# Kernel optimization log

Hardware: AMD Instinct MI355X
Metric: run time of the kernel (lower is better)

## Reference

```python
import jax, jax.numpy as jnp
import numpy as np
import math

PATCH = 41
NUM_ANG = 8
NUM_SPATIAL = 4
BIN_KSIZE = 2 * int(PATCH / (NUM_SPATIAL + 1))   # 16
BIN_STRIDE = PATCH // NUM_SPATIAL                # 10
BIN_PAD = BIN_KSIZE // 4                         # 4
CLIPVAL = 0.2
EPS = 1e-10
N = 8192


def _sift_pooling_kernel(ksize: int) -> np.ndarray:
    k2 = float(ksize) / 2.0
    xc2 = k2 - np.abs(np.arange(ksize, dtype=np.float32) + 0.5 - k2)
    return (np.outer(xc2, xc2) / k2 ** 2).astype(np.float32)


def _sift_weighting_kernel(ksize: int) -> np.ndarray:
    # Gauss, vlfeat sigma: sigma_mul_2 = ksize**2
    k2 = float(ksize) / 2.0
    ys = np.arange(ksize, dtype=np.float32)[:, None]
    xs = np.arange(ksize, dtype=np.float32)[None, :]
    disq = (ys - k2 + 0.5) ** 2 + (xs - k2 + 0.5) ** 2
    return np.exp(-disq / float(ksize ** 2)).astype(np.float32)


def setup_inputs() -> dict:
    key = jax.random.key(0)
    x = jax.random.normal(key, (N, 1, PATCH, PATCH), dtype=jnp.float32)
    gk = jnp.asarray(_sift_weighting_kernel(PATCH))   # [41,41]
    pk = jnp.asarray(_sift_pooling_kernel(BIN_KSIZE))  # [16,16]
    return {"x": x, "gk": gk, "pk": pk}


def _l2_normalize(v):
    return v / jnp.maximum(jnp.linalg.norm(v, axis=1, keepdims=True), 1e-12)


def reference(x, gk, pk):
    # gradients via replicate-pad + central difference (matches [-1,0,1] convs)
    xp = jnp.pad(x, ((0, 0), (0, 0), (0, 0), (1, 1)), mode='edge')
    gx = xp[..., 2:] - xp[..., :-2]
    yp = jnp.pad(x, ((0, 0), (0, 0), (1, 1), (0, 0)), mode='edge')
    gy = yp[:, :, 2:, :] - yp[:, :, :-2, :]

    mag = jnp.sqrt(gx * gx + gy * gy + EPS) * gk  # gaussian-weighted magnitude
    ori = jnp.arctan2(gy, gx + EPS)

    # soft angular binning
    o_big = (ori + 2.0 * math.pi) / (2.0 * math.pi) * NUM_ANG
    bo0f = jnp.floor(o_big)
    wo1 = o_big - bo0f
    bo0 = bo0f.astype(jnp.int32) % NUM_ANG
    bo1 = (bo0 + 1) % NUM_ANG
    # [N,1,P,P,nb]
    contrib = (jax.nn.one_hot(bo0, NUM_ANG, dtype=mag.dtype) * ((1.0 - wo1) * mag)[..., None]
               + jax.nn.one_hot(bo1, NUM_ANG, dtype=mag.dtype) * (wo1 * mag)[..., None])
    contrib = jnp.transpose(contrib[:, 0], (0, 3, 1, 2))  # [N,nb,P,P]

    # depthwise weighted spatial pooling (same triangular kernel per angular bin)
    kern = jnp.broadcast_to(pk[None, None], (NUM_ANG, 1, BIN_KSIZE, BIN_KSIZE))
    pooled = jax.lax.conv_general_dilated(
        contrib, kern,
        window_strides=(BIN_STRIDE, BIN_STRIDE),
        padding=[(BIN_PAD, BIN_PAD), (BIN_PAD, BIN_PAD)],
        feature_group_count=NUM_ANG,
        dimension_numbers=('NCHW', 'OIHW', 'NCHW'))  # [N,nb,4,4]

    desc = pooled.reshape(pooled.shape[0], -1)  # [N,128]
    desc = _l2_normalize(desc)
    desc = jnp.clip(desc, 0.0, CLIPVAL)
    desc = _l2_normalize(desc)
    # rootsift: sqrt of L1-normalized descriptor
    desc = desc / jnp.maximum(jnp.sum(jnp.abs(desc), axis=1, keepdims=True), 1e-12)
    return jnp.sqrt(desc + 1e-10)
```

## Files before the change

### kernel.cpp

```cpp
#include <hip/hip_runtime.h>
#include <hip/hip_fp16.h>
#include <math.h>

#define PATCH 41
#define PP 1681
#define NB 8
#define STRIDE 10
#define PAD 4
#define NTH 192
#define XROW 52
#define XSZ (PATCH * XROW)

__device__ __forceinline__ constexpr float tri16(int k) {
    float d = (float)k + 0.5f - 8.0f;
    float a = d < 0.0f ? -d : d;
    return (8.0f - a) * 0.125f;
}

__device__ __forceinline__ uint4 pixel_contrib(float gx, float gy, float gauss) {
    float X = gx + 1e-10f;
    float mag = __builtin_amdgcn_sqrtf(fmaf(gx, gx, fmaf(gy, gy, 1e-10f))) * gauss;

    float ax = fabsf(X), ay = fabsf(gy);
    float mx = fmaxf(ax, ay), mn = fminf(ax, ay);
    float r = mn * __builtin_amdgcn_rcpf(fmaxf(mx, 1e-30f));
    float r2 = r * r;
    float a4 = fmaf(r2, -0.0149238f, 0.0670406f);
    a4 = fmaf(r2, a4, -0.1482457f);
    a4 = fmaf(r2, a4, 0.2464287f);
    a4 = fmaf(r2, a4, -0.4235106f);
    a4 = fmaf(r2, a4, 1.2732106f);
    a4 *= r;

    bool sw = ay > ax;
    bool xn = X < 0.0f;
    bool yn = gy < 0.0f;
    int q = (xn ? 2 : 0) + ((sw != xn) ? 1 : 0);
    int b0 = yn ? 7 - q : q;
    bool f = (sw != xn) != yn;
    float ma = a4 * mag;
    float mb = mag - ma;
    float v0 = f ? ma : mb;
    float v1 = f ? mb : ma;

    unsigned combo = __builtin_bit_cast(unsigned, __builtin_amdgcn_cvt_pkrtz(v0, v1));
    int sh = (b0 & 3) << 4;
    unsigned long long A = (unsigned long long)combo << sh;
    unsigned long long B = ((b0 & 3) == 3) ? (unsigned long long)(combo >> 16) : 0ull;
    bool lohalf = b0 < 4;
    unsigned long long lo = lohalf ? A : B;
    unsigned long long hi = lohalf ? B : A;
    uint4 cw;
    cw.x = (unsigned)lo; cw.y = (unsigned)(lo >> 32);
    cw.z = (unsigned)hi; cw.w = (unsigned)(hi >> 32);
    return cw;
}

__global__ __launch_bounds__(NTH, 6) void sift_desc_kernel(
        const float* __restrict__ x,
        const float* __restrict__ gk,
        const float* __restrict__ pk,
        float* __restrict__ out)
{
    const int patch = blockIdx.x;
    const int t = threadIdx.x;

    __shared__ __align__(16) __half s_xp[XSZ];
    __shared__ __align__(16) __half s_cw[XROW];
    __shared__ __align__(16) __half s_H[PATCH * 4 * NB];
    __shared__ float s_desc[128];

    const float* xp = x + (size_t)patch * PP;
    for (int idx = t; idx < XSZ; idx += NTH) {
        int i = idx / XROW;
        int c = idx - i * XROW - 6;
        int jc = min(max(c, 0), PATCH - 1);
        s_xp[idx] = __float2half(xp[i * PATCH + jc]);
    }
    if (t < XROW) {
        float dj = (float)(t - 26);
        s_cw[t] = __float2half(__builtin_amdgcn_exp2f(dj * dj * -8.582362e-4f));
    }
    __syncthreads();

    if (t < PATCH * 4) {
        const int row = t >> 2;
        const int ox = t & 3;
        const int jw0 = ox * STRIDE - PAD;
        const int base = jw0 + 6;
        const int rowM = row * XROW;
        const int rowU = (row > 0 ? row - 1 : 0) * XROW;
        const int rowD = (row < PATCH - 1 ? row + 1 : PATCH - 1) * XROW;
        const bool zlo = (ox == 0);
        const bool zhi = (ox == 3);

        float drow = (float)(row - 20);
        const float rf = __builtin_amdgcn_exp2f(drow * drow * -8.582362e-4f);

        __half2 pmh = *(const __half2*)&s_xp[rowM + base - 2];
        __half2 cmh = *(const __half2*)&s_xp[rowM + base];
        float pm0 = __low2float(pmh), pm1 = __high2float(pmh);
        float cm0 = __low2float(cmh), cm1 = __high2float(cmh);

        const __half2 z2 = __float2half2_rn(0.0f);
        __half2 a0 = z2, a1 = z2, a2 = z2, a3 = z2;

        #pragma unroll
        for (int it = 0; it < 8; ++it) {
            const int kx0 = 2 * it;
            __half2 nmh = *(const __half2*)&s_xp[rowM + base + kx0 + 2];
            __half2 uh  = *(const __half2*)&s_xp[rowU + base + kx0];
            __half2 dh  = *(const __half2*)&s_xp[rowD + base + kx0];
            __half2 cwh = *(const __half2*)&s_cw[base + kx0];

            __half2 gyh = __hsub2(dh, uh);
            float gy0 = __low2float(gyh), gy1 = __high2float(gyh);
            float nm0 = __low2float(nmh), nm1 = __high2float(nmh);
            float cf0 = __low2float(cwh), cf1 = __high2float(cwh);

            float w0 = tri16(kx0);
            float w1 = tri16(kx0 + 1);
            if (kx0 < 4)      { w0 = zlo ? 0.0f : w0; w1 = zlo ? 0.0f : w1; }
            if (kx0 + 1 == 15){ w1 = zhi ? 0.0f : w1; }

            uint4 c0 = pixel_contrib(cm1 - pm1, gy0, rf * (w0 * cf0));
            uint4 c1 = pixel_contrib(nm0 - cm0, gy1, rf * (w1 * cf1));

            a0 = __hadd2(a0, __hadd2(*(__half2*)&c0.x, *(__half2*)&c1.x));
            a1 = __hadd2(a1, __hadd2(*(__half2*)&c0.y, *(__half2*)&c1.y));
            a2 = __hadd2(a2, __hadd2(*(__half2*)&c0.z, *(__half2*)&c1.z));
            a3 = __hadd2(a3, __hadd2(*(__half2*)&c0.w, *(__half2*)&c1.w));

            pm0 = cm0; pm1 = cm1;
            cm0 = nm0; cm1 = nm1;
        }

        uint4 hv;
        hv.x = *(unsigned*)&a0;
        hv.y = *(unsigned*)&a1;
        hv.z = *(unsigned*)&a2;
        hv.w = *(unsigned*)&a3;
        *(uint4*)&s_H[(row * 4 + ox) * NB] = hv;
    }
    __syncthreads();

    if (t < 128) {
        int b = t >> 4;
        int oy = (t >> 2) & 3;
        int ox = t & 3;
        float v = 0.0f;
        #pragma unroll
        for (int ky = 0; ky < 16; ++ky) {
            const float w = tri16(ky);
            int iy = oy * STRIDE - PAD + ky;
            int iyc = min(max(iy, 0), PATCH - 1);
            float hv = __half2float(s_H[(iyc * 4 + ox) * NB + b]);
            v = fmaf((iy == iyc) ? w : 0.0f, hv, v);
        }
        s_desc[t] = v;
    }
    __syncthreads();

    if (t < 64) {
        float a = s_desc[t];
        float b = s_desc[t + 64];

        float ss = fmaf(a, a, b * b);
        #pragma unroll
        for (int o = 32; o > 0; o >>= 1) ss += __shfl_xor(ss, o);
        float inv = 1.0f / fmaxf(__builtin_amdgcn_sqrtf(ss), 1e-12f);
        a = fminf(fmaxf(a * inv, 0.0f), 0.2f);
        b = fminf(fmaxf(b * inv, 0.0f), 0.2f);

        float ss2 = fmaf(a, a, b * b);
        #pragma unroll
        for (int o = 32; o > 0; o >>= 1) ss2 += __shfl_xor(ss2, o);
        float inv2 = 1.0f / fmaxf(__builtin_amdgcn_sqrtf(ss2), 1e-12f);
        a *= inv2; b *= inv2;

        float l1 = a + b;
        #pragma unroll
        for (int o = 32; o > 0; o >>= 1) l1 += __shfl_xor(l1, o);
        float invl = 1.0f / fmaxf(l1, 1e-12f);

        float* op = out + (size_t)patch * 128;
        op[t]      = __builtin_amdgcn_sqrtf(fmaf(a, invl, 1e-10f));
        op[t + 64] = __builtin_amdgcn_sqrtf(fmaf(b, invl, 1e-10f));
    }
}

extern "C" void kernel_launch(void* const* d_in, const int* in_sizes, int n_in,
                              void* d_out, int out_size, void* d_ws, size_t ws_size,
                              hipStream_t stream) {
    const float* x  = (const float*)d_in[0];
    const float* gk = (const float*)d_in[1];
    const float* pk = (const float*)d_in[2];
    float* out = (float*)d_out;
    const int n = in_sizes[0] / PP;
    sift_desc_kernel<<<n, NTH, 0, stream>>>(x, gk, pk, out);
}
```

Measured before the change: 125.3 us.

## Store patch as fp32 in LDS, precompute column weights, zero-pad row histogram

```diff
diff --git a/kernel.cpp b/kernel.cpp
--- a/kernel.cpp
+++ b/kernel.cpp
@@ -8,8 +8,8 @@
 #define STRIDE 10
 #define PAD 4
 #define NTH 192
-#define XROW 52
-#define XSZ (PATCH * XROW)
+#define XR 50
+#define HR 5
 
 __device__ __forceinline__ constexpr float tri16(int k) {
     float d = (float)k + 0.5f - 8.0f;
@@ -17,9 +17,9 @@
     return (8.0f - a) * 0.125f;
 }
 
-__device__ __forceinline__ uint4 pixel_contrib(float gx, float gy, float gauss) {
+__device__ __forceinline__ uint4 pixel_contrib(float gx, float gy, float w) {
     float X = gx + 1e-10f;
-    float mag = __builtin_amdgcn_sqrtf(fmaf(gx, gx, fmaf(gy, gy, 1e-10f))) * gauss;
+    float mag = __builtin_amdgcn_sqrtf(fmaf(gx, gx, fmaf(gy, gy, 1e-10f))) * w;
 
     float ax = fabsf(X), ay = fabsf(gy);
     float mx = fmaxf(ax, ay), mn = fminf(ax, ay);
@@ -65,42 +65,60 @@
     const int patch = blockIdx.x;
     const int t = threadIdx.x;
 
-    __shared__ __align__(16) __half s_xp[XSZ];
-    __shared__ __align__(16) __half s_cw[XROW];
-    __shared__ __align__(16) __half s_H[PATCH * 4 * NB];
+    __shared__ __align__(16) float s_xp[PATCH * XR];
+    __shared__ __align__(16) float s_wl[64];
+    __shared__ __align__(16) __half s_H[49 * HR * NB];
     __shared__ float s_desc[128];
 
     const float* xp = x + (size_t)patch * PP;
-    for (int idx = t; idx < XSZ; idx += NTH) {
-        int i = idx / XROW;
-        int c = idx - i * XROW - 6;
-        int jc = min(max(c, 0), PATCH - 1);
-        s_xp[idx] = __float2half(xp[i * PATCH + jc]);
-    }
-    if (t < XROW) {
-        float dj = (float)(t - 26);
-        s_cw[t] = __float2half(__builtin_amdgcn_exp2f(dj * dj * -8.582362e-4f));
+    for (int p = t; p < PP; p += NTH) {
+        int i = p / PATCH;
+        int j = p - i * PATCH;
+        s_xp[i * XR + j + 6] = xp[p];
+    }
+    for (int q = t; q < 41 * 9; q += NTH) {
+        int i = q / 9;
+        int c = q - i * 9;
+        int j = (c < 6) ? (c - 6) : (c + 35);
+        int jc = min(max(j, 0), PATCH - 1);
+        s_xp[i * XR + j + 6] = xp[i * PATCH + jc];
+    }
+    if (t < 64) {
+        int ox = t >> 4, kx = t & 15;
+        int col = ox * STRIDE - PAD + kx;
+        float d = (float)(col - 20);
+        float g = __builtin_amdgcn_exp2f(d * d * -8.582362e-4f);
+        bool oob = (col < 0) | (col > PATCH - 1);
+        s_wl[t] = oob ? 0.0f : tri16(kx) * g;
+    }
+    if (t < 160) {
+        int dw = (t < 80) ? t : (820 + t);
+        ((unsigned*)s_H)[dw] = 0u;
     }
     __syncthreads();
 
     if (t < PATCH * 4) {
         const int row = t >> 2;
         const int ox = t & 3;
-        const int jw0 = ox * STRIDE - PAD;
-        const int base = jw0 + 6;
-        const int rowM = row * XROW;
-        const int rowU = (row > 0 ? row - 1 : 0) * XROW;
-        const int rowD = (row < PATCH - 1 ? row + 1 : PATCH - 1) * XROW;
-        const bool zlo = (ox == 0);
-        const bool zhi = (ox == 3);
+        const int rowM = row * XR + ox * STRIDE + 2;
+        const int rowU = (row > 0 ? row - 1 : 0) * XR + ox * STRIDE + 2;
+        const int rowD = (row < PATCH - 1 ? row + 1 : PATCH - 1) * XR + ox * STRIDE + 2;
 
         float drow = (float)(row - 20);
         const float rf = __builtin_amdgcn_exp2f(drow * drow * -8.582362e-4f);
 
-        __half2 pmh = *(const __half2*)&s_xp[rowM + base - 2];
-        __half2 cmh = *(const __half2*)&s_xp[rowM + base];
-        float pm0 = __low2float(pmh), pm1 = __high2float(pmh);
-        float cm0 = __low2float(cmh), cm1 = __high2float(cmh);
+        float wf[16];
+        {
+            const float4* wl4 = (const float4*)&s_wl[ox << 4];
+            float4 w0 = wl4[0], w1 = wl4[1], w2 = wl4[2], w3 = wl4[3];
+            wf[0] = w0.x * rf;  wf[1] = w0.y * rf;  wf[2] = w0.z * rf;  wf[3] = w0.w * rf;
+            wf[4] = w1.x * rf;  wf[5] = w1.y * rf;  wf[6] = w1.z * rf;  wf[7] = w1.w * rf;
+            wf[8] = w2.x * rf;  wf[9] = w2.y * rf;  wf[10] = w2.z * rf; wf[11] = w2.w * rf;
+            wf[12] = w3.x * rf; wf[13] = w3.y * rf; wf[14] = w3.z * rf; wf[15] = w3.w * rf;
+        }
+
+        float2 pm = *(const float2*)&s_xp[rowM - 2];
+        float2 cm = *(const float2*)&s_xp[rowM];
 
         const __half2 z2 = __float2half2_rn(0.0f);
         __half2 a0 = z2, a1 = z2, a2 = z2, a3 = z2;
@@ -108,31 +126,20 @@
         #pragma unroll
         for (int it = 0; it < 8; ++it) {
             const int kx0 = 2 * it;
-            __half2 nmh = *(const __half2*)&s_xp[rowM + base + kx0 + 2];
-            __half2 uh  = *(const __half2*)&s_xp[rowU + base + kx0];
-            __half2 dh  = *(const __half2*)&s_xp[rowD + base + kx0];
-            __half2 cwh = *(const __half2*)&s_cw[base + kx0];
-
-            __half2 gyh = __hsub2(dh, uh);
-            float gy0 = __low2float(gyh), gy1 = __high2float(gyh);
-            float nm0 = __low2float(nmh), nm1 = __high2float(nmh);
-            float cf0 = __low2float(cwh), cf1 = __high2float(cwh);
-
-            float w0 = tri16(kx0);
-            float w1 = tri16(kx0 + 1);
-            if (kx0 < 4)      { w0 = zlo ? 0.0f : w0; w1 = zlo ? 0.0f : w1; }
-            if (kx0 + 1 == 15){ w1 = zhi ? 0.0f : w1; }
-
-            uint4 c0 = pixel_contrib(cm1 - pm1, gy0, rf * (w0 * cf0));
-            uint4 c1 = pixel_contrib(nm0 - cm0, gy1, rf * (w1 * cf1));
+            float2 nm = *(const float2*)&s_xp[rowM + kx0 + 2];
+            float2 uu = *(const float2*)&s_xp[rowU + kx0];
+            float2 dd = *(const float2*)&s_xp[rowD + kx0];
+
+            uint4 c0 = pixel_contrib(cm.y - pm.y, dd.x - uu.x, wf[kx0]);
+            uint4 c1 = pixel_contrib(nm.x - cm.x, dd.y - uu.y, wf[kx0 + 1]);
 
             a0 = __hadd2(a0, __hadd2(*(__half2*)&c0.x, *(__half2*)&c1.x));
             a1 = __hadd2(a1, __hadd2(*(__half2*)&c0.y, *(__half2*)&c1.y));
             a2 = __hadd2(a2, __hadd2(*(__half2*)&c0.z, *(__half2*)&c1.z));
             a3 = __hadd2(a3, __hadd2(*(__half2*)&c0.w, *(__half2*)&c1.w));
 
-            pm0 = cm0; pm1 = cm1;
-            cm0 = nm0; cm1 = nm1;
+            pm = cm;
+            cm = nm;
         }
 
         uint4 hv;
@@ -140,7 +147,7 @@
         hv.y = *(unsigned*)&a1;
         hv.z = *(unsigned*)&a2;
         hv.w = *(unsigned*)&a3;
-        *(uint4*)&s_H[(row * 4 + ox) * NB] = hv;
+        *(uint4*)&s_H[((row + 4) * HR + ox) * NB] = hv;
     }
     __syncthreads();
 
@@ -148,14 +155,11 @@
         int b = t >> 4;
         int oy = (t >> 2) & 3;
         int ox = t & 3;
+        const __half* hp = &s_H[(oy * STRIDE * HR + ox) * NB + b];
         float v = 0.0f;
         #pragma unroll
         for (int ky = 0; ky < 16; ++ky) {
-            const float w = tri16(ky);
-            int iy = oy * STRIDE - PAD + ky;
-            int iyc = min(max(iy, 0), PATCH - 1);
-            float hv = __half2float(s_H[(iyc * 4 + ox) * NB + b]);
-            v = fmaf((iy == iyc) ? w : 0.0f, hv, v);
+            v = fmaf(tri16(ky), __half2float(hp[ky * HR * NB]), v);
         }
         s_desc[t] = v;
     }
```

Result: faster. 120.2 us (-4.0%).
